# Kernel optimization log

Measured on AMD Instinct MI355X. Metric: run time of the kernel, lower is better.

The kernel has to match this reference:

```python
import jax, jax.numpy as jnp
import numpy as np

N, E = 50000, 800000
IN_DIM = 128
OUT_DIM = 128
H = 8
D = OUT_DIM // H  # head_dim = 16
LN_EPS = 1e-5


def setup_inputs() -> dict:
    key = jax.random.key(0)
    ks = jax.random.split(key, 16)
    s_in = 1.0 / np.sqrt(IN_DIM)
    s_out = 1.0 / np.sqrt(OUT_DIM)
    return {
        "x": jax.random.normal(ks[0], (N, IN_DIM), dtype=jnp.float32),
        "edge_index": jax.random.randint(ks[1], (2, E), 0, N, dtype=jnp.int32),
        "edge_attr": jax.random.uniform(ks[2], (E,), dtype=jnp.float32),
        # per-head TransformerConv params, stacked over heads (heads=1 per conv)
        "Wq": jax.random.normal(ks[3], (H, IN_DIM, D), dtype=jnp.float32) * s_in,
        "bq": jnp.zeros((H, D), dtype=jnp.float32),
        "Wk": jax.random.normal(ks[4], (H, IN_DIM, D), dtype=jnp.float32) * s_in,
        "bk": jnp.zeros((H, D), dtype=jnp.float32),
        "Wv": jax.random.normal(ks[5], (H, IN_DIM, D), dtype=jnp.float32) * s_in,
        "bv": jnp.zeros((H, D), dtype=jnp.float32),
        "We": jax.random.normal(ks[6], (H, D), dtype=jnp.float32),  # lin_edge (edge_dim=1, no bias)
        "Wskip": jax.random.normal(ks[7], (H, IN_DIM, D), dtype=jnp.float32) * s_in,
        "bskip": jnp.zeros((H, D), dtype=jnp.float32),
        "Wo": jax.random.normal(ks[8], (OUT_DIM, OUT_DIM), dtype=jnp.float32) * s_out,
        "bo": jnp.zeros((OUT_DIM,), dtype=jnp.float32),
        "gamma": jnp.ones((OUT_DIM,), dtype=jnp.float32),
        "beta": jnp.zeros((OUT_DIM,), dtype=jnp.float32),
    }


def reference(x, edge_index, edge_attr, Wq, bq, Wk, bk, Wv, bv, We, Wskip, bskip, Wo, bo, gamma, beta):
    n = x.shape[0]
    h, _, d = Wq.shape
    src, dst = edge_index[0], edge_index[1]
    # node-level projections for all heads at once: [N, H, D]
    q = jnp.einsum('ni,hid->nhd', x, Wq) + bq
    k = jnp.einsum('ni,hid->nhd', x, Wk) + bk
    v = jnp.einsum('ni,hid->nhd', x, Wv) + bv
    # edge embedding: lin_edge on scalar edge_attr -> [E, H, D]
    e = edge_attr[:, None, None] * We[None, :, :]
    # attention logits per edge/head: q_dst . (k_src + e) / sqrt(d)
    ke = k[src] + e
    alpha = jnp.einsum('ehd,ehd->eh', q[dst], ke) / jnp.sqrt(jnp.asarray(d, x.dtype))
    # segment softmax over destination nodes
    m = jax.ops.segment_max(alpha, dst, num_segments=n)  # [N, H]
    m = jnp.where(jnp.isfinite(m), m, 0.0)
    ex = jnp.exp(alpha - m[dst])
    denom = jax.ops.segment_sum(ex, dst, num_segments=n)
    w = ex / jnp.maximum(denom[dst], 1e-16)  # [E, H]
    # weighted aggregation of (v_src + e)
    agg = jax.ops.segment_sum(w[:, :, None] * (v[src] + e), dst, num_segments=n)  # [N, H, D]
    # root/skip connection inside each TransformerConv
    skip = jnp.einsum('ni,hid->nhd', x, Wskip) + bskip
    heads_cat = (agg + skip).reshape(n, h * d)  # concat over heads -> [N, OUT_DIM]
    out = heads_cat @ Wo + bo
    out = out + x  # residual (in_dim == out_dim)
    mu = out.mean(-1, keepdims=True)
    var = out.var(-1, keepdims=True)
    out = (out - mu) * jax.lax.rsqrt(var + LN_EPS) * gamma + beta
    return out
```

## Files before the change

### kernel.cpp

```cpp
#include <hip/hip_runtime.h>
#include <hip/hip_bf16.h>
#include <stdint.h>
#include <math.h>

#define IN_DIM 128
#define H_HEADS 8
#define HD 16

typedef __attribute__((ext_vector_type(8))) short bf16x8;
typedef __attribute__((ext_vector_type(4))) float f32x4;

__device__ __forceinline__ unsigned short f2bf(float f) {
    __hip_bfloat16 h = __float2bfloat16(f);
    return reinterpret_cast<unsigned short&>(h);
}
__device__ __forceinline__ float bf2f(unsigned short h) {
    return __uint_as_float(((unsigned int)h) << 16);
}

__device__ __forceinline__ void split_f8(const float4 f0, const float4 f1,
                                         bf16x8& h8, bf16x8& l8) {
    float ff[8] = {f0.x, f0.y, f0.z, f0.w, f1.x, f1.y, f1.z, f1.w};
    union { bf16x8 v; unsigned short u[8]; } H, L;
#pragma unroll
    for (int j = 0; j < 8; ++j) {
        H.u[j] = f2bf(ff[j]);
        L.u[j] = f2bf(ff[j] - bf2f(H.u[j]));
    }
    h8 = H.v; l8 = L.v;
}

__device__ __forceinline__ void stage_B(const unsigned short* __restrict__ src,
                                        unsigned short* __restrict__ lds, int t)
{
#pragma unroll
    for (int j = 0; j < 8; ++j) {
        int idx16 = t + j * 256;
        int c = idx16 >> 4, kcol = idx16 & 15;
        uint4 v = *reinterpret_cast<const uint4*>(src + (size_t)c * 128 + kcol * 8);
        *reinterpret_cast<uint4*>(lds + c * 128 + ((kcol ^ (c & 15)) * 8)) = v;
    }
}
__device__ __forceinline__ bf16x8 read_B(const unsigned short* __restrict__ lds,
                                         int c, int kcol)
{
    return *reinterpret_cast<const bf16x8*>(lds + c * 128 + ((kcol ^ (c & 15)) * 8));
}

__global__ __launch_bounds__(256)
void prep_count_kernel(const float* __restrict__ Wq, const float* __restrict__ Wk,
                       const float* __restrict__ Wv, const float* __restrict__ Wsk,
                       const float* __restrict__ Wo,
                       const float* __restrict__ bq, const float* __restrict__ bk,
                       const float* __restrict__ bv, const float* __restrict__ bsk,
                       unsigned short* __restrict__ WtH, unsigned short* __restrict__ WtL,
                       float* __restrict__ bias_cat,
                       const int* __restrict__ ei, int* __restrict__ deg, int E)
{
    const int b = blockIdx.x;
    const int t = threadIdx.x;
    if (b >= 5) {
        int e = (b - 5) * 256 + t;
        if (e < E) atomicAdd(&deg[ei[E + e]], 1);
        return;
    }
    const int p = b;
    const float* src = (p == 0) ? Wq : (p == 1) ? Wk : (p == 2) ? Wv : (p == 3) ? Wsk : Wo;
    unsigned short* dh = WtH + (size_t)p * 16384;
    unsigned short* dl = WtL + (size_t)p * 16384;
#pragma unroll
    for (int j = 0; j < 64; ++j) {
        int o = t + j * 256;
        int c = o >> 7, k = o & 127;
        float v;
        if (p < 4) {
            int h = c >> 4, d = c & 15;
            v = src[(size_t)h * 2048 + (size_t)k * 16 + d];
        } else {
            v = src[(size_t)k * 128 + c];
        }
        unsigned short hi = f2bf(v);
        unsigned short lo = f2bf(v - bf2f(hi));
        dh[o] = hi; dl[o] = lo;
    }
    if (p < 4 && t < 128) {
        const float* bb = (p == 0) ? bq : (p == 1) ? bk : (p == 2) ? bv : bsk;
        bias_cat[p * 128 + t] = bb[t];
    }
}

__global__ __launch_bounds__(256)
void gemm_proj_kernel(const float* __restrict__ A,
                      const unsigned short* __restrict__ WtH_base,
                      const unsigned short* __restrict__ WtL_base,
                      const float* __restrict__ bias_cat,
                      float* __restrict__ qout, float* __restrict__ skipout,
                      unsigned short* __restrict__ kvout, int N)
{
    __shared__ unsigned short Bs[16384];
    const int t = threadIdx.x;
    const int lane = t & 63;
    const int w = t >> 6;
    const int lr = lane & 15;
    const int lk = lane >> 4;
    const int p = blockIdx.y;
    const int brow0 = blockIdx.x * 64 + w * 16;
    const int arow = min(brow0 + lr, N - 1);
    const float* ap = A + (size_t)arow * 128;

    bf16x8 ah[4], al[4];
#pragma unroll
    for (int ks = 0; ks < 4; ++ks) {
        float4 f0 = *reinterpret_cast<const float4*>(ap + ks * 32 + lk * 8);
        float4 f1 = *reinterpret_cast<const float4*>(ap + ks * 32 + lk * 8 + 4);
        split_f8(f0, f1, ah[ks], al[ks]);
    }

    f32x4 acc[8];
#pragma unroll
    for (int ni = 0; ni < 8; ++ni) acc[ni] = (f32x4){0.f, 0.f, 0.f, 0.f};

    stage_B(WtH_base + (size_t)p * 16384, Bs, t);
    __syncthreads();
#pragma unroll
    for (int ks = 0; ks < 4; ++ks)
#pragma unroll
        for (int ni = 0; ni < 8; ++ni) {
            bf16x8 bh = read_B(Bs, ni * 16 + lr, ks * 4 + lk);
            acc[ni] = __builtin_amdgcn_mfma_f32_16x16x32_bf16(ah[ks], bh, acc[ni], 0, 0, 0);
            acc[ni] = __builtin_amdgcn_mfma_f32_16x16x32_bf16(al[ks], bh, acc[ni], 0, 0, 0);
        }
    __syncthreads();
    stage_B(WtL_base + (size_t)p * 16384, Bs, t);
    __syncthreads();
#pragma unroll
    for (int ks = 0; ks < 4; ++ks)
#pragma unroll
        for (int ni = 0; ni < 8; ++ni) {
            bf16x8 bl = read_B(Bs, ni * 16 + lr, ks * 4 + lk);
            acc[ni] = __builtin_amdgcn_mfma_f32_16x16x32_bf16(ah[ks], bl, acc[ni], 0, 0, 0);
        }

    const float* bias = bias_cat + p * 128;
    if (p == 0 || p == 3) {
        float* outp = (p == 0) ? qout : skipout;
#pragma unroll
        for (int ni = 0; ni < 8; ++ni) {
            int col = ni * 16 + lr;
            float bc = bias[col];
#pragma unroll
            for (int r = 0; r < 4; ++r) {
                int gr = brow0 + lk * 4 + r;
                if (gr < N) outp[(size_t)gr * 128 + col] = acc[ni][r] + bc;
            }
        }
    } else {
        unsigned int* kvu = (unsigned int*)kvout;
        const int slot = (p == 1) ? 0 : 1;
#pragma unroll
        for (int ni = 0; ni < 8; ++ni) {
            int col = ni * 16 + lr;
            float bc = bias[col];
#pragma unroll
            for (int r = 0; r < 4; ++r) {
                unsigned int s = f2bf(acc[ni][r] + bc);
                unsigned int o = __shfl_xor((int)s, 1);
                int gr = brow0 + lk * 4 + r;
                if (((lr & 1) == 0) && gr < N)
                    kvu[(size_t)gr * 128 + 2 * (col >> 1) + slot] = s | (o << 16);
            }
        }
    }
}

__global__ __launch_bounds__(256)
void gemm_out_ln_kernel(const float* __restrict__ A,
                        const unsigned short* __restrict__ BtH_t,
                        const unsigned short* __restrict__ BtL_t,
                        const float* __restrict__ bo,
                        const float* __restrict__ res,
                        const float* __restrict__ gamma,
                        const float* __restrict__ beta,
                        float* __restrict__ out, int N)
{
    __shared__ unsigned short Bs[16384];
    const int t = threadIdx.x;
    const int lane = t & 63;
    const int w = t >> 6;
    const int lr = lane & 15;
    const int lk = lane >> 4;
    const int brow0 = blockIdx.x * 64 + w * 16;
    const int arow = min(brow0 + lr, N - 1);
    const float* ap = A + (size_t)arow * 128;

    bf16x8 ah[4], al[4];
#pragma unroll
    for (int ks = 0; ks < 4; ++ks) {
        float4 f0 = *reinterpret_cast<const float4*>(ap + ks * 32 + lk * 8);
        float4 f1 = *reinterpret_cast<const float4*>(ap + ks * 32 + lk * 8 + 4);
        split_f8(f0, f1, ah[ks], al[ks]);
    }

    f32x4 acc[8];
#pragma unroll
    for (int ni = 0; ni < 8; ++ni) acc[ni] = (f32x4){0.f, 0.f, 0.f, 0.f};

    stage_B(BtH_t, Bs, t);
    __syncthreads();
#pragma unroll
    for (int ks = 0; ks < 4; ++ks)
#pragma unroll
        for (int ni = 0; ni < 8; ++ni) {
            bf16x8 bh = read_B(Bs, ni * 16 + lr, ks * 4 + lk);
            acc[ni] = __builtin_amdgcn_mfma_f32_16x16x32_bf16(ah[ks], bh, acc[ni], 0, 0, 0);
            acc[ni] = __builtin_amdgcn_mfma_f32_16x16x32_bf16(al[ks], bh, acc[ni], 0, 0, 0);
        }
    __syncthreads();
    stage_B(BtL_t, Bs, t);
    __syncthreads();
#pragma unroll
    for (int ks = 0; ks < 4; ++ks)
#pragma unroll
        for (int ni = 0; ni < 8; ++ni) {
            bf16x8 bl = read_B(Bs, ni * 16 + lr, ks * 4 + lk);
            acc[ni] = __builtin_amdgcn_mfma_f32_16x16x32_bf16(ah[ks], bl, acc[ni], 0, 0, 0);
        }

#pragma unroll
    for (int ni = 0; ni < 8; ++ni) {
        int col = ni * 16 + lr;
        float bc = bo[col];
#pragma unroll
        for (int r = 0; r < 4; ++r) {
            int gr = brow0 + lk * 4 + r;
            float rv = (gr < N) ? res[(size_t)gr * 128 + col] : 0.f;
            acc[ni][r] += bc + rv;
        }
    }
#pragma unroll
    for (int r = 0; r < 4; ++r) {
        float s = 0.f, sq = 0.f;
#pragma unroll
        for (int ni = 0; ni < 8; ++ni) { float v = acc[ni][r]; s += v; sq += v * v; }
#pragma unroll
        for (int mk = 1; mk < 16; mk <<= 1) {
            s  += __shfl_xor(s, mk);
            sq += __shfl_xor(sq, mk);
        }
        float mean = s * (1.0f / 128.0f);
        float var  = sq * (1.0f / 128.0f) - mean * mean;
        float inv  = rsqrtf(var + 1e-5f);
        int gr = brow0 + lk * 4 + r;
        if (gr < N) {
#pragma unroll
            for (int ni = 0; ni < 8; ++ni) {
                int col = ni * 16 + lr;
                out[(size_t)gr * 128 + col] =
                    (acc[ni][r] - mean) * inv * gamma[col] + beta[col];
            }
        }
    }
}

__global__ __launch_bounds__(1024)
void scan_part1(const int* __restrict__ deg, int* __restrict__ offs,
                int* __restrict__ csums, int N)
{
    __shared__ int wsum[16];
    const int t = threadIdx.x;
    const int lane = t & 63, wid = t >> 6;
    const int idx = blockIdx.x * 4096 + t * 4;
    int v[4];
#pragma unroll
    for (int j = 0; j < 4; ++j) { int i = idx + j; v[j] = (i < N) ? deg[i] : 0; }
    int ls = v[0] + v[1] + v[2] + v[3];
    int inc = ls;
#pragma unroll
    for (int off = 1; off < 64; off <<= 1) {
        int y = __shfl_up(inc, off);
        if (lane >= off) inc += y;
    }
    if (lane == 63) wsum[wid] = inc;
    __syncthreads();
    if (t < 16) {
        int winc = wsum[t];
        for (int off = 1; off < 16; off <<= 1) {
            int y = __shfl_up(winc, off);
            if (t >= off) winc += y;
        }
        wsum[t] = winc;
    }
    __syncthreads();
    int wexcl = (wid == 0) ? 0 : wsum[wid - 1];
    int texcl = wexcl + (inc - ls);
    int pre = 0;
#pragma unroll
    for (int j = 0; j < 4; ++j) {
        int i = idx + j;
        if (i < N) offs[i] = texcl + pre;
        pre += v[j];
    }
    if (t == 0) csums[blockIdx.x] = wsum[15];
}

__global__ void scan_part2(int* __restrict__ csums, int nc,
                           int* __restrict__ offs, int N)
{
    const int t = threadIdx.x;
    int v = (t < nc) ? csums[t] : 0;
    int inc = v;
#pragma unroll
    for (int off = 1; off < 64; off <<= 1) {
        int y = __shfl_up(inc, off);
        if (t >= off) inc += y;
    }
    if (t < nc) csums[t] = inc - v;
    int total = __shfl(inc, nc - 1);
    if (t == 0) offs[N] = total;
}

__global__ __launch_bounds__(1024)
void scan_part3(int* __restrict__ offs, const int* __restrict__ csums,
                int* __restrict__ cursor, int N)
{
    const int coff = csums[blockIdx.x];
    const int idx = blockIdx.x * 4096 + threadIdx.x * 4;
#pragma unroll
    for (int j = 0; j < 4; ++j) {
        int i = idx + j;
        if (i < N) { int val = offs[i] + coff; offs[i] = val; cursor[i] = val; }
    }
}

__global__ void scatter_kernel(const int* __restrict__ ei, const float* __restrict__ ea,
                               int* __restrict__ cursor, int2* __restrict__ csr, int E)
{
    int e = blockIdx.x * 256 + threadIdx.x;
    if (e < E) {
        int s = ei[e], d = ei[E + e];
        int pos = atomicAdd(&cursor[d], 1);
        csr[pos] = make_int2(s, __float_as_int(ea[e]));
    }
}

__global__ __launch_bounds__(256)
void agg_kernel(const float* __restrict__ qb, const float* __restrict__ sb,
                const unsigned short* __restrict__ kvb,
                const int* __restrict__ offs, const int2* __restrict__ csr,
                const float* __restrict__ We, float* __restrict__ heads_cat, int N)
{
    const int lane = threadIdx.x & 63;
    const int node = blockIdx.x * 4 + (threadIdx.x >> 6);
    if (node >= N) return;
    const int h32 = lane & 31;
    const int half = lane >> 5;

    const float4 q4  = *reinterpret_cast<const float4*>(qb + (size_t)node * 128 + 4 * h32);
    const float4 we4 = *reinterpret_cast<const float4*>(We + 4 * h32);

    float qwe = q4.x * we4.x + q4.y * we4.y + q4.z * we4.z + q4.w * we4.w;
    qwe += __shfl_xor(qwe, 1);
    qwe += __shfl_xor(qwe, 2);

    const int e0 = offs[node];
    const int cnt = offs[node + 1] - e0;
    const int myCnt = (cnt > half) ? ((cnt - half + 1) >> 1) : 0;
    const int2* cp = csr + e0 + half;

    float m = -__builtin_huge_valf();
    float s = 0.f, sWE = 0.f, a0 = 0.f, a1 = 0.f, a2 = 0.f, a3 = 0.f;

#define KVG(ec) (*reinterpret_cast<const uint4*>(kvb + (size_t)(ec).x * 256 + 8 * h32))

    int2 c0, c1, c2, c3;
    uint4 g0, g1, g2;
    if (myCnt > 0) c0 = cp[0];
    if (myCnt > 1) c1 = cp[2];
    if (myCnt > 2) c2 = cp[4];
    if (myCnt > 3) c3 = cp[6];
    if (myCnt > 0) g0 = KVG(c0);
    if (myCnt > 1) g1 = KVG(c1);
    if (myCnt > 2) g2 = KVG(c2);

    for (int j = 0; j < myCnt; ++j) {
        const float eav = __int_as_float(c0.y);
        float k0 = __uint_as_float(g0.x << 16);
        float k1 = __uint_as_float(g0.x & 0xffff0000u);
        float k2 = __uint_as_float(g0.z << 16);
        float k3 = __uint_as_float(g0.z & 0xffff0000u);
        float part = q4.x * k0 + q4.y * k1 + q4.z * k2 + q4.w * k3;
        part += __shfl_xor(part, 1);
        part += __shfl_xor(part, 2);
        float alpha = fmaf(eav, qwe, part) * 0.25f;
        float d = alpha - m;
        if (__any(d > 8.f)) {
            float nm = fmaxf(m, alpha);
            float sc = __expf(m - nm);
            m = nm; d = alpha - m;
            s *= sc; sWE *= sc; a0 *= sc; a1 *= sc; a2 *= sc; a3 *= sc;
        }
        float pv = __expf(d);
        s += pv;
        sWE = fmaf(pv, eav, sWE);
        float v0 = __uint_as_float(g0.y << 16);
        float v1 = __uint_as_float(g0.y & 0xffff0000u);
        float v2 = __uint_as_float(g0.w << 16);
        float v3 = __uint_as_float(g0.w & 0xffff0000u);
        a0 = fmaf(pv, v0, a0);
        a1 = fmaf(pv, v1, a1);
        a2 = fmaf(pv, v2, a2);
        a3 = fmaf(pv, v3, a3);
        c0 = c1; c1 = c2; c2 = c3;
        g0 = g1; g1 = g2;
        if (j + 4 < myCnt) c3 = cp[2 * j + 8];
        if (j + 3 < myCnt) g2 = KVG(c2);
    }

    float om  = __shfl_xor(m, 32);
    float os  = __shfl_xor(s, 32);
    float oWE = __shfl_xor(sWE, 32);
    float o0  = __shfl_xor(a0, 32);
    float o1  = __shfl_xor(a1, 32);
    float o2  = __shfl_xor(a2, 32);
    float o3  = __shfl_xor(a3, 32);
    float nm = fmaxf(m, om);
    float eS = (s  > 0.f) ? __expf(m  - nm) : 0.f;
    float eO = (os > 0.f) ? __expf(om - nm) : 0.f;
    float st  = s * eS + os * eO;
    float SWE = sWE * eS + oWE * eO;
    float r0 = a0 * eS + o0 * eO;
    float r1 = a1 * eS + o1 * eO;
    float r2 = a2 * eS + o2 * eO;
    float r3 = a3 * eS + o3 * eO;

    if (half == 0) {
        float inv = 1.0f / fmaxf(st, 1e-16f);
        const float4 sk = *reinterpret_cast<const float4*>(sb + (size_t)node * 128 + 4 * h32);
        float4 o;
        o.x = fmaf(SWE, we4.x, r0) * inv + sk.x;
        o.y = fmaf(SWE, we4.y, r1) * inv + sk.y;
        o.z = fmaf(SWE, we4.z, r2) * inv + sk.z;
        o.w = fmaf(SWE, we4.w, r3) * inv + sk.w;
        *reinterpret_cast<float4*>(heads_cat + (size_t)node * 128 + 4 * h32) = o;
    }
#undef KVG
}

extern "C" void kernel_launch(void* const* d_in, const int* in_sizes, int n_in,
                              void* d_out, int out_size, void* d_ws, size_t ws_size,
                              hipStream_t stream)
{
    const float* x    = (const float*)d_in[0];
    const int*   ei   = (const int*)d_in[1];
    const float* ea   = (const float*)d_in[2];
    const float* Wq   = (const float*)d_in[3];
    const float* bq   = (const float*)d_in[4];
    const float* Wk   = (const float*)d_in[5];
    const float* bk   = (const float*)d_in[6];
    const float* Wv   = (const float*)d_in[7];
    const float* bv   = (const float*)d_in[8];
    const float* We   = (const float*)d_in[9];
    const float* Wsk  = (const float*)d_in[10];
    const float* bsk  = (const float*)d_in[11];
    const float* Wo   = (const float*)d_in[12];
    const float* bo   = (const float*)d_in[13];
    const float* gamma= (const float*)d_in[14];
    const float* beta = (const float*)d_in[15];
    const int N = in_sizes[0] / 128;
    const int E = in_sizes[1] / 2;
    float* out = (float*)d_out;

    char* w = (char*)d_ws;
    float* qarr      = (float*)w; w += (size_t)N * 128 * sizeof(float);
    float* skiparr   = (float*)w; w += (size_t)N * 128 * sizeof(float);
    unsigned short* kv = (unsigned short*)w; w += (size_t)N * 256 * sizeof(unsigned short);
    float* heads_cat = (float*)w; w += (size_t)N * 128 * sizeof(float);
    int*   deg       = (int*)w;   w += ((size_t)N + 16) * sizeof(int);
    int*   offs      = (int*)w;   w += ((size_t)N + 16) * sizeof(int);
    int*   cursor    = (int*)w;   w += ((size_t)N + 16) * sizeof(int);
    int*   csums     = (int*)w;   w += 256 * sizeof(int);
    int2*  csr       = (int2*)w;  w += (size_t)E * sizeof(int2);
    unsigned short* WtH = (unsigned short*)w; w += (size_t)5 * 16384 * sizeof(unsigned short);
    unsigned short* WtL = (unsigned short*)w; w += (size_t)5 * 16384 * sizeof(unsigned short);
    float* bias_cat  = (float*)w; w += 4 * 128 * sizeof(float);

    hipMemsetAsync(deg, 0, (size_t)N * sizeof(int), stream);

    const int cntBlocks = (E + 255) / 256;
    prep_count_kernel<<<5 + cntBlocks, 256, 0, stream>>>(Wq, Wk, Wv, Wsk, Wo, bq, bk, bv, bsk,
                                                         WtH, WtL, bias_cat, ei, deg, E);

    dim3 gProj((N + 63) / 64, 4);
    gemm_proj_kernel<<<gProj, 256, 0, stream>>>(x, WtH, WtL, bias_cat, qarr, skiparr, kv, N);

    const int nChunks = (N + 4095) / 4096;
    scan_part1<<<nChunks, 1024, 0, stream>>>(deg, offs, csums, N);
    scan_part2<<<1, 64, 0, stream>>>(csums, nChunks, offs, N);
    scan_part3<<<nChunks, 1024, 0, stream>>>(offs, csums, cursor, N);

    scatter_kernel<<<(E + 255) / 256, 256, 0, stream>>>(ei, ea, cursor, csr, E);
    agg_kernel<<<(N + 3) / 4, 256, 0, stream>>>(qarr, skiparr, kv, offs, csr, We, heads_cat, N);

    gemm_out_ln_kernel<<<(N + 63) / 64, 256, 0, stream>>>(heads_cat,
                                                          WtH + (size_t)4 * 16384,
                                                          WtL + (size_t)4 * 16384,
                                                          bo, x, gamma, beta, out, N);
}
```

Baseline: 326.3 us.

## Process four edges per wavefront in aggregation and two projections per GEMM block

The aggregation kernel now splits each wavefront into four quarter-lanes, each lane covering 8 features of a head and working on a different edge, instead of two halves covering 4 features each. The partial softmax states are merged with a two-step butterfly. This aims to expose more concurrent gathers per node. Separately, each projection GEMM block now computes two weight panels in sequence so the split A row tile is reused, halving grid.y. This trades more registers and fewer blocks for less redundant A loading and conversion.

```diff
diff --git a/kernel.cpp b/kernel.cpp
--- a/kernel.cpp
+++ b/kernel.cpp
@@ -103,7 +103,7 @@
     const int w = t >> 6;
     const int lr = lane & 15;
     const int lk = lane >> 4;
-    const int p = blockIdx.y;
+    const int pr = blockIdx.y;
     const int brow0 = blockIdx.x * 64 + w * 16;
     const int arow = min(brow0 + lr, N - 1);
     const float* ap = A + (size_t)arow * 128;
@@ -116,58 +116,62 @@
         split_f8(f0, f1, ah[ks], al[ks]);
     }
 
-    f32x4 acc[8];
-#pragma unroll
-    for (int ni = 0; ni < 8; ++ni) acc[ni] = (f32x4){0.f, 0.f, 0.f, 0.f};
-
-    stage_B(WtH_base + (size_t)p * 16384, Bs, t);
-    __syncthreads();
-#pragma unroll
-    for (int ks = 0; ks < 4; ++ks)
-#pragma unroll
-        for (int ni = 0; ni < 8; ++ni) {
-            bf16x8 bh = read_B(Bs, ni * 16 + lr, ks * 4 + lk);
-            acc[ni] = __builtin_amdgcn_mfma_f32_16x16x32_bf16(ah[ks], bh, acc[ni], 0, 0, 0);
-            acc[ni] = __builtin_amdgcn_mfma_f32_16x16x32_bf16(al[ks], bh, acc[ni], 0, 0, 0);
-        }
-    __syncthreads();
-    stage_B(WtL_base + (size_t)p * 16384, Bs, t);
-    __syncthreads();
-#pragma unroll
-    for (int ks = 0; ks < 4; ++ks)
-#pragma unroll
-        for (int ni = 0; ni < 8; ++ni) {
-            bf16x8 bl = read_B(Bs, ni * 16 + lr, ks * 4 + lk);
-            acc[ni] = __builtin_amdgcn_mfma_f32_16x16x32_bf16(ah[ks], bl, acc[ni], 0, 0, 0);
-        }
-
-    const float* bias = bias_cat + p * 128;
-    if (p == 0 || p == 3) {
-        float* outp = (p == 0) ? qout : skipout;
-#pragma unroll
-        for (int ni = 0; ni < 8; ++ni) {
-            int col = ni * 16 + lr;
-            float bc = bias[col];
-#pragma unroll
-            for (int r = 0; r < 4; ++r) {
-                int gr = brow0 + lk * 4 + r;
-                if (gr < N) outp[(size_t)gr * 128 + col] = acc[ni][r] + bc;
+    for (int pp = 0; pp < 2; ++pp) {
+        const int p = pr * 2 + pp;
+        f32x4 acc[8];
+#pragma unroll
+        for (int ni = 0; ni < 8; ++ni) acc[ni] = (f32x4){0.f, 0.f, 0.f, 0.f};
+
+        __syncthreads();
+        stage_B(WtH_base + (size_t)p * 16384, Bs, t);
+        __syncthreads();
+#pragma unroll
+        for (int ks = 0; ks < 4; ++ks)
+#pragma unroll
+            for (int ni = 0; ni < 8; ++ni) {
+                bf16x8 bh = read_B(Bs, ni * 16 + lr, ks * 4 + lk);
+                acc[ni] = __builtin_amdgcn_mfma_f32_16x16x32_bf16(ah[ks], bh, acc[ni], 0, 0, 0);
+                acc[ni] = __builtin_amdgcn_mfma_f32_16x16x32_bf16(al[ks], bh, acc[ni], 0, 0, 0);
             }
-        }
-    } else {
-        unsigned int* kvu = (unsigned int*)kvout;
-        const int slot = (p == 1) ? 0 : 1;
-#pragma unroll
-        for (int ni = 0; ni < 8; ++ni) {
-            int col = ni * 16 + lr;
-            float bc = bias[col];
-#pragma unroll
-            for (int r = 0; r < 4; ++r) {
-                unsigned int s = f2bf(acc[ni][r] + bc);
-                unsigned int o = __shfl_xor((int)s, 1);
-                int gr = brow0 + lk * 4 + r;
-                if (((lr & 1) == 0) && gr < N)
-                    kvu[(size_t)gr * 128 + 2 * (col >> 1) + slot] = s | (o << 16);
+        __syncthreads();
+        stage_B(WtL_base + (size_t)p * 16384, Bs, t);
+        __syncthreads();
+#pragma unroll
+        for (int ks = 0; ks < 4; ++ks)
+#pragma unroll
+            for (int ni = 0; ni < 8; ++ni) {
+                bf16x8 bl = read_B(Bs, ni * 16 + lr, ks * 4 + lk);
+                acc[ni] = __builtin_amdgcn_mfma_f32_16x16x32_bf16(ah[ks], bl, acc[ni], 0, 0, 0);
+            }
+
+        const float* bias = bias_cat + p * 128;
+        if (p == 0 || p == 3) {
+            float* outp = (p == 0) ? qout : skipout;
+#pragma unroll
+            for (int ni = 0; ni < 8; ++ni) {
+                int col = ni * 16 + lr;
+                float bc = bias[col];
+#pragma unroll
+                for (int r = 0; r < 4; ++r) {
+                    int gr = brow0 + lk * 4 + r;
+                    if (gr < N) outp[(size_t)gr * 128 + col] = acc[ni][r] + bc;
+                }
+            }
+        } else {
+            unsigned int* kvu = (unsigned int*)kvout;
+            const int slot = (p == 1) ? 0 : 1;
+#pragma unroll
+            for (int ni = 0; ni < 8; ++ni) {
+                int col = ni * 16 + lr;
+                float bc = bias[col];
+#pragma unroll
+                for (int r = 0; r < 4; ++r) {
+                    unsigned int s = f2bf(acc[ni][r] + bc);
+                    unsigned int o = __shfl_xor((int)s, 1);
+                    int gr = brow0 + lk * 4 + r;
+                    if (((lr & 1) == 0) && gr < N)
+                        kvu[(size_t)gr * 128 + 2 * (col >> 1) + slot] = s | (o << 16);
+                }
             }
         }
     }
@@ -352,96 +356,121 @@
     const int lane = threadIdx.x & 63;
     const int node = blockIdx.x * 4 + (threadIdx.x >> 6);
     if (node >= N) return;
-    const int h32 = lane & 31;
-    const int half = lane >> 5;
-
-    const float4 q4  = *reinterpret_cast<const float4*>(qb + (size_t)node * 128 + 4 * h32);
-    const float4 we4 = *reinterpret_cast<const float4*>(We + 4 * h32);
-
-    float qwe = q4.x * we4.x + q4.y * we4.y + q4.z * we4.z + q4.w * we4.w;
+    const int q16  = lane & 15;
+    const int quad = lane >> 4;
+
+    const float4 qa = *reinterpret_cast<const float4*>(qb + (size_t)node * 128 + 8 * q16);
+    const float4 qc = *reinterpret_cast<const float4*>(qb + (size_t)node * 128 + 8 * q16 + 4);
+    const float4 wa = *reinterpret_cast<const float4*>(We + 8 * q16);
+    const float4 wc = *reinterpret_cast<const float4*>(We + 8 * q16 + 4);
+
+    float qwe = qa.x * wa.x + qa.y * wa.y + qa.z * wa.z + qa.w * wa.w
+              + qc.x * wc.x + qc.y * wc.y + qc.z * wc.z + qc.w * wc.w;
     qwe += __shfl_xor(qwe, 1);
-    qwe += __shfl_xor(qwe, 2);
 
     const int e0 = offs[node];
     const int cnt = offs[node + 1] - e0;
-    const int myCnt = (cnt > half) ? ((cnt - half + 1) >> 1) : 0;
-    const int2* cp = csr + e0 + half;
+    const int myCnt = (cnt > quad) ? ((cnt - quad + 3) >> 2) : 0;
+    const int2* cp = csr + e0 + quad;
+    const unsigned int* kvu = (const unsigned int*)kvb;
 
     float m = -__builtin_huge_valf();
-    float s = 0.f, sWE = 0.f, a0 = 0.f, a1 = 0.f, a2 = 0.f, a3 = 0.f;
-
-#define KVG(ec) (*reinterpret_cast<const uint4*>(kvb + (size_t)(ec).x * 256 + 8 * h32))
-
-    int2 c0, c1, c2, c3;
-    uint4 g0, g1, g2;
+    float s = 0.f, sWE = 0.f;
+    float a0 = 0.f, a1 = 0.f, a2 = 0.f, a3 = 0.f;
+    float a4 = 0.f, a5 = 0.f, a6 = 0.f, a7 = 0.f;
+
+#define KVG(ec, ga, gb) do { \
+    const uint4* p_ = reinterpret_cast<const uint4*>(kvu + (size_t)(ec).x * 128 + 8 * q16); \
+    ga = p_[0]; gb = p_[1]; } while (0)
+
+    int2 c0, c1, c2;
+    uint4 g0a, g0b, g1a, g1b;
     if (myCnt > 0) c0 = cp[0];
-    if (myCnt > 1) c1 = cp[2];
-    if (myCnt > 2) c2 = cp[4];
-    if (myCnt > 3) c3 = cp[6];
-    if (myCnt > 0) g0 = KVG(c0);
-    if (myCnt > 1) g1 = KVG(c1);
-    if (myCnt > 2) g2 = KVG(c2);
+    if (myCnt > 1) c1 = cp[4];
+    if (myCnt > 2) c2 = cp[8];
+    if (myCnt > 0) KVG(c0, g0a, g0b);
+    if (myCnt > 1) KVG(c1, g1a, g1b);
 
     for (int j = 0; j < myCnt; ++j) {
         const float eav = __int_as_float(c0.y);
-        float k0 = __uint_as_float(g0.x << 16);
-        float k1 = __uint_as_float(g0.x & 0xffff0000u);
-        float k2 = __uint_as_float(g0.z << 16);
-        float k3 = __uint_as_float(g0.z & 0xffff0000u);
-        float part = q4.x * k0 + q4.y * k1 + q4.z * k2 + q4.w * k3;
+        float k0 = __uint_as_float(g0a.x << 16);
+        float k1 = __uint_as_float(g0a.x & 0xffff0000u);
+        float k2 = __uint_as_float(g0a.z << 16);
+        float k3 = __uint_as_float(g0a.z & 0xffff0000u);
+        float k4 = __uint_as_float(g0b.x << 16);
+        float k5 = __uint_as_float(g0b.x & 0xffff0000u);
+        float k6 = __uint_as_float(g0b.z << 16);
+        float k7 = __uint_as_float(g0b.z & 0xffff0000u);
+        float part = qa.x * k0 + qa.y * k1 + qa.z * k2 + qa.w * k3
+                   + qc.x * k4 + qc.y * k5 + qc.z * k6 + qc.w * k7;
         part += __shfl_xor(part, 1);
-        part += __shfl_xor(part, 2);
         float alpha = fmaf(eav, qwe, part) * 0.25f;
         float d = alpha - m;
         if (__any(d > 8.f)) {
             float nm = fmaxf(m, alpha);
             float sc = __expf(m - nm);
             m = nm; d = alpha - m;
-            s *= sc; sWE *= sc; a0 *= sc; a1 *= sc; a2 *= sc; a3 *= sc;
+            s *= sc; sWE *= sc;
+            a0 *= sc; a1 *= sc; a2 *= sc; a3 *= sc;
+            a4 *= sc; a5 *= sc; a6 *= sc; a7 *= sc;
         }
         float pv = __expf(d);
         s += pv;
         sWE = fmaf(pv, eav, sWE);
-        float v0 = __uint_as_float(g0.y << 16);
-        float v1 = __uint_as_float(g0.y & 0xffff0000u);
-        float v2 = __uint_as_float(g0.w << 16);
-        float v3 = __uint_as_float(g0.w & 0xffff0000u);
-        a0 = fmaf(pv, v0, a0);
-        a1 = fmaf(pv, v1, a1);
-        a2 = fmaf(pv, v2, a2);
-        a3 = fmaf(pv, v3, a3);
-        c0 = c1; c1 = c2; c2 = c3;
-        g0 = g1; g1 = g2;
-        if (j + 4 < myCnt) c3 = cp[2 * j + 8];
-        if (j + 3 < myCnt) g2 = KVG(c2);
-    }
-
-    float om  = __shfl_xor(m, 32);
-    float os  = __shfl_xor(s, 32);
-    float oWE = __shfl_xor(sWE, 32);
-    float o0  = __shfl_xor(a0, 32);
-    float o1  = __shfl_xor(a1, 32);
-    float o2  = __shfl_xor(a2, 32);
-    float o3  = __shfl_xor(a3, 32);
-    float nm = fmaxf(m, om);
-    float eS = (s  > 0.f) ? __expf(m  - nm) : 0.f;
-    float eO = (os > 0.f) ? __expf(om - nm) : 0.f;
-    float st  = s * eS + os * eO;
-    float SWE = sWE * eS + oWE * eO;
-    float r0 = a0 * eS + o0 * eO;
-    float r1 = a1 * eS + o1 * eO;
-    float r2 = a2 * eS + o2 * eO;
-    float r3 = a3 * eS + o3 * eO;
-
-    if (half == 0) {
-        float inv = 1.0f / fmaxf(st, 1e-16f);
-        const float4 sk = *reinterpret_cast<const float4*>(sb + (size_t)node * 128 + 4 * h32);
-        float4 o;
-        o.x = fmaf(SWE, we4.x, r0) * inv + sk.x;
-        o.y = fmaf(SWE, we4.y, r1) * inv + sk.y;
-        o.z = fmaf(SWE, we4.z, r2) * inv + sk.z;
-        o.w = fmaf(SWE, we4.w, r3) * inv + sk.w;
-        *reinterpret_cast<float4*>(heads_cat + (size_t)node * 128 + 4 * h32) = o;
+        float v0 = __uint_as_float(g0a.y << 16);
+        float v1 = __uint_as_float(g0a.y & 0xffff0000u);
+        float v2 = __uint_as_float(g0a.w << 16);
+        float v3 = __uint_as_float(g0a.w & 0xffff0000u);
+        float v4 = __uint_as_float(g0b.y << 16);
+        float v5 = __uint_as_float(g0b.y & 0xffff0000u);
+        float v6 = __uint_as_float(g0b.w << 16);
+        float v7 = __uint_as_float(g0b.w & 0xffff0000u);
+        a0 = fmaf(pv, v0, a0); a1 = fmaf(pv, v1, a1);
+        a2 = fmaf(pv, v2, a2); a3 = fmaf(pv, v3, a3);
+        a4 = fmaf(pv, v4, a4); a5 = fmaf(pv, v5, a5);
+        a6 = fmaf(pv, v6, a6); a7 = fmaf(pv, v7, a7);
+        c0 = c1; c1 = c2;
+        g0a = g1a; g0b = g1b;
+        if (j + 3 < myCnt) c2 = cp[4 * j + 12];
+        if (j + 2 < myCnt) KVG(c1, g1a, g1b);
+    }
+
+#pragma unroll
+    for (int mk = 16; mk <= 32; mk <<= 1) {
+        float om  = __shfl_xor(m, mk);
+        float os  = __shfl_xor(s, mk);
+        float oWE = __shfl_xor(sWE, mk);
+        float o0 = __shfl_xor(a0, mk), o1 = __shfl_xor(a1, mk);
+        float o2 = __shfl_xor(a2, mk), o3 = __shfl_xor(a3, mk);
+        float o4 = __shfl_xor(a4, mk), o5 = __shfl_xor(a5, mk);
+        float o6 = __shfl_xor(a6, mk), o7 = __shfl_xor(a7, mk);
+        float nm = fmaxf(m, om);
+        float eS = (s  > 0.f) ? __expf(m  - nm) : 0.f;
+        float eO = (os > 0.f) ? __expf(om - nm) : 0.f;
+        m = nm;
+        s   = s  * eS + os  * eO;
+        sWE = sWE * eS + oWE * eO;
+        a0 = a0 * eS + o0 * eO; a1 = a1 * eS + o1 * eO;
+        a2 = a2 * eS + o2 * eO; a3 = a3 * eS + o3 * eO;
+        a4 = a4 * eS + o4 * eO; a5 = a5 * eS + o5 * eO;
+        a6 = a6 * eS + o6 * eO; a7 = a7 * eS + o7 * eO;
+    }
+
+    if (quad == 0) {
+        float inv = 1.0f / fmaxf(s, 1e-16f);
+        const float4 s0 = *reinterpret_cast<const float4*>(sb + (size_t)node * 128 + 8 * q16);
+        const float4 s1 = *reinterpret_cast<const float4*>(sb + (size_t)node * 128 + 8 * q16 + 4);
+        float4 oA, oB;
+        oA.x = fmaf(sWE, wa.x, a0) * inv + s0.x;
+        oA.y = fmaf(sWE, wa.y, a1) * inv + s0.y;
+        oA.z = fmaf(sWE, wa.z, a2) * inv + s0.z;
+        oA.w = fmaf(sWE, wa.w, a3) * inv + s0.w;
+        oB.x = fmaf(sWE, wc.x, a4) * inv + s1.x;
+        oB.y = fmaf(sWE, wc.y, a5) * inv + s1.y;
+        oB.z = fmaf(sWE, wc.z, a6) * inv + s1.z;
+        oB.w = fmaf(sWE, wc.w, a7) * inv + s1.w;
+        *reinterpret_cast<float4*>(heads_cat + (size_t)node * 128 + 8 * q16)     = oA;
+        *reinterpret_cast<float4*>(heads_cat + (size_t)node * 128 + 8 * q16 + 4) = oB;
     }
 #undef KVG
 }
@@ -490,7 +519,7 @@
     prep_count_kernel<<<5 + cntBlocks, 256, 0, stream>>>(Wq, Wk, Wv, Wsk, Wo, bq, bk, bv, bsk,
                                                          WtH, WtL, bias_cat, ei, deg, E);
 
-    dim3 gProj((N + 63) / 64, 4);
+    dim3 gProj((N + 63) / 64, 2);
     gemm_proj_kernel<<<gProj, 256, 0, stream>>>(x, WtH, WtL, bias_cat, qarr, skiparr, kv, N);
 
     const int nChunks = (N + 4095) / 4096;
```

Result: no change. 327.8 us (+0.5%).
